# Performance work log

Measured on AMD Instinct MI355X. Metric: run time of the kernel, lower is better.

Reference implementation:

```python
import jax, jax.numpy as jnp
import numpy as np

VOCAB = 100000
EMB = 128
B = 16384
C = 20
N = 20


def setup_inputs() -> dict:
    key = jax.random.key(0)
    k1, k2, k3, k4, k5 = jax.random.split(key, 5)
    initrange = 1.0 / EMB
    return {
        "pos_target": jax.random.randint(k1, (B,), 0, VOCAB),
        "pos_contexts": jax.random.randint(k2, (B, C), 0, VOCAB),
        "pos_negatives": jax.random.randint(k3, (B, N), 0, VOCAB),
        "context_table": jax.random.uniform(k4, (VOCAB, EMB), jnp.float32, -initrange, initrange),
        "output_table": jax.random.uniform(k5, (VOCAB, EMB), jnp.float32, -initrange, initrange),
    }


def reference(pos_target, pos_contexts, pos_negatives, context_table, output_table):
    # gather + sum over context window: [B, C, D] -> [B, D]
    mean_contexts = jnp.sum(context_table[pos_contexts], axis=1)
    emb_target = output_table[pos_target]           # [B, D]
    emb_negs = output_table[pos_negatives]          # [B, N, D]

    # positive objective: dot(mean_contexts, emb_target) per row
    pos_score = jnp.clip(jnp.sum(mean_contexts * emb_target, axis=1), -10.0, 10.0)
    objective = -jax.nn.log_sigmoid(pos_score)      # [B]

    # negative objective: bmm [B,N,D] x [B,D] -> [B,N]
    neg_score = jnp.clip(jnp.einsum("bnd,bd->bn", emb_negs, mean_contexts), -10.0, 10.0)
    neg_objective = -jnp.sum(jax.nn.log_sigmoid(-neg_score), axis=1)  # [B]

    return jnp.mean(objective + neg_objective)
```

## Files before the change

kernel.cpp:

```cpp
#include <hip/hip_runtime.h>
#include <math.h>

#define VOCAB 100000
#define EMB   128
#define BATCH 16384
#define CTX   20
#define NEG   20

__global__ void zero_out_kernel(float* out) {
    out[0] = 0.0f;
}

__device__ __forceinline__ float half_wave_dot(float4 a, float4 b) {
    float p = a.x * b.x + a.y * b.y + a.z * b.z + a.w * b.w;
    p += __shfl_xor(p, 16);
    p += __shfl_xor(p, 8);
    p += __shfl_xor(p, 4);
    p += __shfl_xor(p, 2);
    p += __shfl_xor(p, 1);
    return p;
}

__global__ __launch_bounds__(256) void cbow_loss_kernel(
    const int*   __restrict__ pos_target,
    const int*   __restrict__ pos_contexts,
    const int*   __restrict__ pos_negatives,
    const float* __restrict__ context_table,
    const float* __restrict__ output_table,
    float*       __restrict__ out)
{
    const int tid  = threadIdx.x;
    const int lane = tid & 63;
    const int wave = tid >> 6;
    const int half = lane >> 5;
    const int sub  = lane & 31;

    const int row = blockIdx.x * 8 + wave * 2 + half;

    const float4* ctab = (const float4*)context_table;
    const float4* otab = (const float4*)output_table;

    float4 acc = make_float4(0.f, 0.f, 0.f, 0.f);
#pragma unroll
    for (int c = 0; c < CTX; ++c) {
        const int idx = pos_contexts[row * CTX + c];
        const float4 v = otab == nullptr ? make_float4(0,0,0,0) : ctab[idx * 32 + sub];
        acc.x += v.x; acc.y += v.y; acc.z += v.z; acc.w += v.w;
    }

    const int t = pos_target[row];
    const float4 et = otab[t * 32 + sub];
    float ps = half_wave_dot(acc, et);
    ps = fminf(fmaxf(ps, -10.f), 10.f);
    float loss = log1pf(expf(-ps));

#pragma unroll
    for (int n = 0; n < NEG; ++n) {
        const int idx = pos_negatives[row * NEG + n];
        const float4 ev = otab[idx * 32 + sub];
        float ns = half_wave_dot(acc, ev);
        ns = fminf(fmaxf(ns, -10.f), 10.f);
        loss += log1pf(expf(ns));
    }

    __shared__ float sdata[8];
    if (sub == 0) sdata[wave * 2 + half] = loss;
    __syncthreads();
    if (tid == 0) {
        float s = 0.f;
#pragma unroll
        for (int i = 0; i < 8; ++i) s += sdata[i];
        atomicAdd(out, s * (1.0f / (float)BATCH));
    }
}

extern "C" void kernel_launch(void* const* d_in, const int* in_sizes, int n_in,
                              void* d_out, int out_size, void* d_ws, size_t ws_size,
                              hipStream_t stream) {
    const int*   pos_target    = (const int*)d_in[0];
    const int*   pos_contexts  = (const int*)d_in[1];
    const int*   pos_negatives = (const int*)d_in[2];
    const float* context_table = (const float*)d_in[3];
    const float* output_table  = (const float*)d_in[4];
    float* out = (float*)d_out;

    zero_out_kernel<<<1, 1, 0, stream>>>(out);

    const int rows_per_block = 8;
    const int grid = BATCH / rows_per_block;
    cbow_loss_kernel<<<grid, 256, 0, stream>>>(
        pos_target, pos_contexts, pos_negatives, context_table, output_table, out);
}
```

Measured before the change: 175.1 us.

## Batch output-table gathers and interleave shuffle reductions across all scores

Restructures the score phase to load target and negative indices up front, then issue the output-table row gathers in groups of seven before computing partial dot products. The butterfly shuffle reductions are interleaved across all 21 scores instead of being done serially per score. It also switches to fast __expf/__logf softplus, adds a launch-bounds occupancy hint, and replaces the zeroing kernel with hipMemsetAsync. The goal is more memory-level parallelism on the gathers, shorter dependent shuffle chains, and fewer launches, at the cost of higher register pressure and slightly reduced accuracy in the transcendentals.

```diff
diff --git a/kernel.cpp b/kernel.cpp
--- a/kernel.cpp
+++ b/kernel.cpp
@@ -6,22 +6,17 @@
 #define BATCH 16384
 #define CTX   20
 #define NEG   20
+#define NSCORE (NEG + 1)
 
-__global__ void zero_out_kernel(float* out) {
-    out[0] = 0.0f;
+__device__ __forceinline__ float dot4(float4 a, float4 b) {
+    return fmaf(a.x, b.x, fmaf(a.y, b.y, fmaf(a.z, b.z, a.w * b.w)));
 }
 
-__device__ __forceinline__ float half_wave_dot(float4 a, float4 b) {
-    float p = a.x * b.x + a.y * b.y + a.z * b.z + a.w * b.w;
-    p += __shfl_xor(p, 16);
-    p += __shfl_xor(p, 8);
-    p += __shfl_xor(p, 4);
-    p += __shfl_xor(p, 2);
-    p += __shfl_xor(p, 1);
-    return p;
+__device__ __forceinline__ float fast_softplus(float x) {
+    return __logf(1.0f + __expf(x));
 }
 
-__global__ __launch_bounds__(256) void cbow_loss_kernel(
+__global__ __launch_bounds__(256, 4) void cbow_loss_kernel(
     const int*   __restrict__ pos_target,
     const int*   __restrict__ pos_contexts,
     const int*   __restrict__ pos_negatives,
@@ -41,26 +36,42 @@
     const float4* otab = (const float4*)output_table;
 
     float4 acc = make_float4(0.f, 0.f, 0.f, 0.f);
+    const int cbase = row * CTX;
 #pragma unroll
     for (int c = 0; c < CTX; ++c) {
-        const int idx = pos_contexts[row * CTX + c];
-        const float4 v = otab == nullptr ? make_float4(0,0,0,0) : ctab[idx * 32 + sub];
+        const int idx = pos_contexts[cbase + c];
+        const float4 v = ctab[idx * 32 + sub];
         acc.x += v.x; acc.y += v.y; acc.z += v.z; acc.w += v.w;
     }
 
-    const int t = pos_target[row];
-    const float4 et = otab[t * 32 + sub];
-    float ps = half_wave_dot(acc, et);
-    ps = fminf(fmaxf(ps, -10.f), 10.f);
-    float loss = log1pf(expf(-ps));
+    int sidx[NSCORE];
+    sidx[0] = pos_target[row];
+    const int nbase = row * NEG;
+#pragma unroll
+    for (int n = 0; n < NEG; ++n) sidx[1 + n] = pos_negatives[nbase + n];
+
+    float part[NSCORE];
+#pragma unroll
+    for (int g = 0; g < 3; ++g) {
+        float4 vb[7];
+#pragma unroll
+        for (int j = 0; j < 7; ++j) vb[j] = otab[sidx[g * 7 + j] * 32 + sub];
+#pragma unroll
+        for (int j = 0; j < 7; ++j) part[g * 7 + j] = dot4(acc, vb[j]);
+    }
 
 #pragma unroll
-    for (int n = 0; n < NEG; ++n) {
-        const int idx = pos_negatives[row * NEG + n];
-        const float4 ev = otab[idx * 32 + sub];
-        float ns = half_wave_dot(acc, ev);
-        ns = fminf(fmaxf(ns, -10.f), 10.f);
-        loss += log1pf(expf(ns));
+    for (int s = 16; s >= 1; s >>= 1) {
+#pragma unroll
+        for (int n = 0; n < NSCORE; ++n) part[n] += __shfl_xor(part[n], s);
+    }
+
+    float ps = fminf(fmaxf(part[0], -10.f), 10.f);
+    float loss = fast_softplus(-ps);
+#pragma unroll
+    for (int n = 1; n < NSCORE; ++n) {
+        float ns = fminf(fmaxf(part[n], -10.f), 10.f);
+        loss += fast_softplus(ns);
     }
 
     __shared__ float sdata[8];
@@ -84,7 +95,7 @@
     const float* output_table  = (const float*)d_in[4];
     float* out = (float*)d_out;
 
-    zero_out_kernel<<<1, 1, 0, stream>>>(out);
+    hipMemsetAsync(out, 0, sizeof(float), stream);
 
     const int rows_per_block = 8;
     const int grid = BATCH / rows_per_block;
```

Result: faster. 151.4 us (-13.6%).
